# Kernel tuning notes

Measured on AMD Instinct MI355X. Metric: run time of the kernel, lower is better.

## Reference

```python
import jax, jax.numpy as jnp
import numpy as np

# Production-scale dims (see shape_source)
L, H, W = 8, 1536, 1536            # layers, grid height, grid width
C = 12                              # number of inter-layer connections
MAX_DIST, TAU = 5, 2.0              # LocalConnectivity distance kernel
DECAY, THRESH, BETA = 0.9, 0.0, 10.0  # SpikeNode params (decay_rate, spike_threshold, surrogate_beta)

# fixed connection topology (src_layer -> dst_layer), mirrors init connections list
_PAIRS = [(0,1),(1,2),(2,3),(3,4),(4,5),(5,6),(6,7),(0,2),(2,4),(4,6),(7,0),(3,5)]


def _distance_kernel():
    ks = 2 * MAX_DIST + 1
    yy, xx = np.meshgrid(np.arange(ks) - MAX_DIST, np.arange(ks) - MAX_DIST, indexing='ij')
    dist = np.sqrt(yy.astype(np.float64) ** 2 + xx.astype(np.float64) ** 2)
    kern = np.exp(-dist / TAU)
    kern[dist > MAX_DIST] = 0.0
    kern[MAX_DIST, MAX_DIST] = 0.0  # no self-connection
    return jnp.asarray(kern, jnp.float32)


def setup_inputs() -> dict:
    key = jax.random.key(0)
    k1, k2, k3, k4, k5 = jax.random.split(key, 5)
    external = jax.random.normal(k1, (L, H, W), jnp.float32)
    prev_spikes = (jax.random.uniform(k2, (L, H, W)) < 0.1).astype(jnp.float32)
    membrane = jax.random.normal(k3, (L, H, W), jnp.float32) * 0.5
    refractory = jax.random.randint(k4, (L, H, W), 0, 4).astype(jnp.int32)
    inter_weights = jax.random.normal(k5, (C, H, W), jnp.float32) * 0.1
    conn_src = jnp.asarray([p[0] for p in _PAIRS], jnp.int32)
    conn_dst = jnp.asarray([p[1] for p in _PAIRS], jnp.int32)
    return {
        'external': external,
        'prev_spikes': prev_spikes,
        'membrane': membrane,
        'inter_weights': inter_weights,
        'local_kernel': _distance_kernel(),
        'refractory': refractory,
        'conn_src': conn_src,
        'conn_dst': conn_dst,
    }


def reference(external, prev_spikes, membrane, inter_weights, local_kernel,
              refractory, conn_src, conn_dst):
    # --- LocalConnectivity: distance-decay lateral conv on previous spikes ---
    # treat L as batch, single channel; SAME padding keeps [L,H,W]
    internal = jax.lax.conv_general_dilated(
        prev_spikes[:, None, :, :], local_kernel[None, None, :, :],
        window_strides=(1, 1), padding='SAME')[:, 0]

    # --- inter-layer axonal input: sum over connections into each dst layer ---
    contrib = prev_spikes[conn_src] * inter_weights          # [C,H,W]
    axonal = jax.ops.segment_sum(contrib, conn_dst, num_segments=L)  # [L,H,W]

    # --- SpikeNode single CLK step (LIF + refractory + surrogate spike) ---
    total = external + internal + axonal
    active = (refractory == 0).astype(total.dtype)           # not in refractory period
    v_new = DECAY * membrane + active * total
    surr = jax.nn.sigmoid(BETA * (v_new - THRESH))           # surrogate (for grads)
    hard = (v_new > THRESH).astype(total.dtype)              # hard Heaviside forward
    spikes = (hard + surr - jax.lax.stop_gradient(surr)) * active  # straight-through
    return spikes
```

## Files before the change

kernel.cpp:

```cpp
#include <hip/hip_runtime.h>
#include <cmath>

namespace {

constexpr int L = 8, H = 1536, W = 1536, HW = H * W, C = 12;
constexpr int TWB = 128, TH = 16;
constexpr int LH = TH + 10;
constexpr int LPAD = 8;
constexpr int LCOLS = 148;

__device__ __host__ constexpr int XLO[11]  = {5, 2, 1, 1, 1, 0, 1, 1, 1, 2, 5};
__device__ __host__ constexpr int XHI[11]  = {5, 8, 9, 9, 9,10, 9, 9, 9, 8, 5};
__device__ __host__ constexpr int WOFF[11] = {0, 1, 8,17,26,35,46,55,64,73,80};

__device__ constexpr int CSRC[C] = {0,1,2,3,4,5,6,0,2,4,7,3};
__device__ constexpr int CDST[C] = {1,2,3,4,5,6,7,2,4,6,0,5};

struct Weights { float w[81]; };

__global__ __launch_bounds__(256)
void snn_fast(const float* __restrict__ ext,
              const float* __restrict__ spk,
              const float* __restrict__ mem,
              const float* __restrict__ iw,
              const int*   __restrict__ refr,
              float* __restrict__ out,
              unsigned*    wslist,
              unsigned     cap,
              const Weights wt)
{
    __shared__ float tile[LH][LCOLS];

    const int tx = threadIdx.x;
    const int ty = threadIdx.y;
    const int tid = ty * 32 + tx;
    const int bx = blockIdx.x, by = blockIdx.y, l = blockIdx.z;

    const int gx0 = bx * TWB - LPAD;
    const int gy0 = by * TH - 5;
    const float* sp_l = spk + l * HW;
    for (int idx = tid; idx < LH * 36; idx += 256) {
        const int r    = idx / 36;
        const int slot = idx - r * 36;
        const int gy = gy0 + r;
        const int gx = gx0 + 4 * slot;
        float4 v = make_float4(0.f, 0.f, 0.f, 0.f);
        if ((unsigned)gy < (unsigned)H) {
            const float* src = sp_l + gy * W;
            if (gx >= 0 && gx + 3 < W) {
                v = *(const float4*)(src + gx);
            } else {
                float t0 = 0.f, t1 = 0.f, t2 = 0.f, t3 = 0.f;
                if ((unsigned)(gx + 0) < (unsigned)W) t0 = src[gx + 0];
                if ((unsigned)(gx + 1) < (unsigned)W) t1 = src[gx + 1];
                if ((unsigned)(gx + 2) < (unsigned)W) t2 = src[gx + 2];
                if ((unsigned)(gx + 3) < (unsigned)W) t3 = src[gx + 3];
                v = make_float4(t0, t1, t2, t3);
            }
        }
        *(float4*)&tile[r][4 * slot] = v;
    }
    __syncthreads();

    float acc[2][4] = {{0.f,0.f,0.f,0.f},{0.f,0.f,0.f,0.f}};
    #pragma unroll
    for (int j = 0; j < 12; ++j) {
        const float* row = &tile[ty * 2 + j][0];
        alignas(16) float win[20];
        *(float4*)&win[0]  = *(const float4*)&row[4 * tx + 0];
        *(float4*)&win[4]  = *(const float4*)&row[4 * tx + 4];
        *(float4*)&win[8]  = *(const float4*)&row[4 * tx + 8];
        *(float4*)&win[12] = *(const float4*)&row[4 * tx + 12];
        win[16] = row[4 * tx + 16];
        #pragma unroll
        for (int k = 0; k < 2; ++k) {
            const int dy = j - k;
            if (dy < 0 || dy > 10) continue;
            #pragma unroll
            for (int dx = XLO[dy]; dx <= XHI[dy]; ++dx) {
                const float wv = wt.w[WOFF[dy] + dx - XLO[dy]];
                #pragma unroll
                for (int c = 0; c < 4; ++c)
                    acc[k][c] += wv * win[3 + c + dx];
            }
        }
    }

    const int ox = bx * TWB + 4 * tx;
    #pragma unroll
    for (int k = 0; k < 2; ++k) {
        const int oy   = by * TH + ty * 2 + k;
        const int pidx = oy * W + ox;
        const int gidx = l * HW + pidx;

        const int4   rf4 = *(const int4*)  (refr + gidx);
        const float4 e4  = *(const float4*)(ext  + gidx);
        const float4 m4  = *(const float4*)(mem  + gidx);

        float ax0 = 0.f, ax1 = 0.f, ax2 = 0.f, ax3 = 0.f;
        #pragma unroll
        for (int c = 0; c < C; ++c) {
            if (CDST[c] != l) continue;
            const float4 s4 = *(const float4*)(spk + CSRC[c] * HW + pidx);
            const float4 w4 = *(const float4*)(iw  + c       * HW + pidx);
            ax0 += s4.x * w4.x; ax1 += s4.y * w4.y;
            ax2 += s4.z * w4.z; ax3 += s4.w * w4.w;
        }
        const float ee[4] = {e4.x, e4.y, e4.z, e4.w};
        const float mm[4] = {m4.x, m4.y, m4.z, m4.w};
        const int   rr[4] = {rf4.x, rf4.y, rf4.z, rf4.w};
        const float aa[4] = {ax0, ax1, ax2, ax3};
        float res[4];
        #pragma unroll
        for (int c = 0; c < 4; ++c) {
            const float v = 0.9f * mm[c] + (ee[c] + acc[k][c] + aa[c]);
            res[c] = (rr[c] == 0 && v > 0.f) ? 1.f : 0.f;
            if (rr[c] == 0 && __builtin_expect(fabsf(v) < 1e-3f, 0)) {
                const unsigned idx = atomicAdd(wslist, 1u);
                if (idx < cap) wslist[1 + idx] = (unsigned)(gidx + c);
            }
        }
        *(float4*)(out + gidx) = make_float4(res[0], res[1], res[2], res[3]);
    }
}

__global__ __launch_bounds__(256)
void snn_fixup(const float* __restrict__ ext,
               const float* __restrict__ spk,
               const float* __restrict__ mem,
               const float* __restrict__ iw,
               const float* __restrict__ lk,
               float* __restrict__ out,
               const unsigned* __restrict__ wslist,
               unsigned cap)
{
    const unsigned n = min(wslist[0], cap);
    for (unsigned i = blockIdx.x * blockDim.x + threadIdx.x; i < n;
         i += gridDim.x * blockDim.x) {
        const unsigned gidx = wslist[1 + i];
        const int l    = gidx / HW;
        const int pidx = gidx - l * HW;
        const int oy   = pidx / W;
        const int ox   = pidx - oy * W;

        const float* sp = spk + l * HW;
        double conv = 0.0;
        for (int dy = 0; dy < 11; ++dy) {
            const int yy = oy + dy - 5;
            if ((unsigned)yy >= (unsigned)H) continue;
            for (int dx = 0; dx < 11; ++dx) {
                const int xx = ox + dx - 5;
                if ((unsigned)xx >= (unsigned)W) continue;
                conv += (double)lk[dy * 11 + dx] * (double)sp[yy * W + xx];
            }
        }
        double ax = 0.0;
        #pragma unroll
        for (int c = 0; c < C; ++c)
            if (CDST[c] == l)
                ax += (double)spk[CSRC[c] * HW + pidx] * (double)iw[c * HW + pidx];
        const double tot = ((double)ext[gidx] + conv) + ax;
        const double vd  = 0.9 * (double)mem[gidx] + tot;
        out[gidx] = (vd > 0.0) ? 1.f : 0.f;
    }
}

}

extern "C" void kernel_launch(void* const* d_in, const int* in_sizes, int n_in,
                              void* d_out, int out_size, void* d_ws, size_t ws_size,
                              hipStream_t stream) {
    const float* ext  = (const float*)d_in[0];
    const float* spk  = (const float*)d_in[1];
    const float* mem  = (const float*)d_in[2];
    const float* iw   = (const float*)d_in[3];
    const float* lk   = (const float*)d_in[4];
    const int*   refr = (const int*)  d_in[5];
    float* o = (float*)d_out;

    Weights wt;
    for (int dy = 0; dy < 11; ++dy) {
        for (int dx = XLO[dy]; dx <= XHI[dy]; ++dx) {
            const double ddy = dy - 5, ddx = dx - 5;
            const double dist = std::sqrt(ddy * ddy + ddx * ddx);
            double w = std::exp(-dist / 2.0);
            if (dist > 5.0) w = 0.0;
            if (dy == 5 && dx == 5) w = 0.0;
            wt.w[WOFF[dy] + dx - XLO[dy]] = (float)w;
        }
    }

    dim3 grid(W / TWB, H / TH, L);
    dim3 block(32, 8, 1);

    unsigned* wsl = (unsigned*)d_ws;
    size_t cap64 = ws_size / 4 - 1;
    const unsigned cap = (unsigned)(cap64 > 0x7FFFFFFFu ? 0x7FFFFFFFu : cap64);
    hipMemsetAsync(d_ws, 0, 4, stream);
    hipLaunchKernelGGL(snn_fast, grid, block, 0, stream,
                       ext, spk, mem, iw, refr, o, wsl, cap, wt);
    hipLaunchKernelGGL(snn_fixup, dim3(64), dim3(256), 0, stream,
                       ext, spk, mem, iw, lk, o, wsl, cap);
}
```

Measured before the change: 188.8 us.

## Compute lateral convolution with bf16 MFMA using hi/lo split weights

Replaces the scalar FP32 11x11 stencil with matrix-core MFMA instructions. Spike tiles are stored as bf16, which is exact for binary spikes, and the kernel weights are split into bf16 high and low parts to keep near-fp32 accuracy. Each block builds banded Toeplitz B matrices in shared memory from the kernel input, and results pass through LDS for the elementwise epilogue. Tiles shrink to 64x16 with one output float4 per thread, which adds per-block weight-setup cost and more halo overhead.

```diff
diff --git a/kernel.cpp b/kernel.cpp
--- a/kernel.cpp
+++ b/kernel.cpp
@@ -1,127 +1,146 @@
 #include <hip/hip_runtime.h>
+#include <hip/hip_bf16.h>
 #include <cmath>
 
 namespace {
 
 constexpr int L = 8, H = 1536, W = 1536, HW = H * W, C = 12;
-constexpr int TWB = 128, TH = 16;
-constexpr int LH = TH + 10;
-constexpr int LPAD = 8;
-constexpr int LCOLS = 148;
-
-__device__ __host__ constexpr int XLO[11]  = {5, 2, 1, 1, 1, 0, 1, 1, 1, 2, 5};
-__device__ __host__ constexpr int XHI[11]  = {5, 8, 9, 9, 9,10, 9, 9, 9, 8, 5};
-__device__ __host__ constexpr int WOFF[11] = {0, 1, 8,17,26,35,46,55,64,73,80};
+constexpr int BTW = 64, BTH = 16;
+constexpr int TROWS = 26;
+constexpr int TCOLS = 88;
+constexpr int NS4 = 22;
 
 __device__ constexpr int CSRC[C] = {0,1,2,3,4,5,6,0,2,4,7,3};
 __device__ constexpr int CDST[C] = {1,2,3,4,5,6,7,2,4,6,0,5};
 
-struct Weights { float w[81]; };
+typedef __attribute__((ext_vector_type(8))) short bf16x8;
+typedef __attribute__((ext_vector_type(4))) float f32x4;
+
+__device__ __forceinline__ short f2b(float x) {
+    __hip_bfloat16 h = __float2bfloat16(x);
+    return *(short*)&h;
+}
 
 __global__ __launch_bounds__(256)
 void snn_fast(const float* __restrict__ ext,
               const float* __restrict__ spk,
               const float* __restrict__ mem,
               const float* __restrict__ iw,
+              const float* __restrict__ lk,
               const int*   __restrict__ refr,
               float* __restrict__ out,
               unsigned*    wslist,
-              unsigned     cap,
-              const Weights wt)
+              unsigned     cap)
 {
-    __shared__ float tile[LH][LCOLS];
-
-    const int tx = threadIdx.x;
-    const int ty = threadIdx.y;
-    const int tid = ty * 32 + tx;
+    __shared__ short Bhi[11 * 512];
+    __shared__ short Blo[11 * 512];
+    __shared__ short tile[TROWS * TCOLS];
+    __shared__ float accb[4 * 256];
+
+    const int tid = threadIdx.x;
+    const int wv  = tid >> 6;
+    const int ln  = tid & 63;
     const int bx = blockIdx.x, by = blockIdx.y, l = blockIdx.z;
 
-    const int gx0 = bx * TWB - LPAD;
-    const int gy0 = by * TH - 5;
+    for (int i = tid; i < 11 * 512; i += 256) {
+        const int dy   = i >> 9;
+        const int r    = i & 511;
+        const int lane = r >> 3, e = r & 7;
+        const int n = lane & 15;
+        const int k = ((lane >> 4) << 3) + e;
+        const int dx = k - n - 3;
+        float w = 0.f;
+        if (dx >= 0 && dx <= 10) w = lk[dy * 11 + dx];
+        const __hip_bfloat16 hb = __float2bfloat16(w);
+        const float rest = w - __bfloat162float(hb);
+        Bhi[i] = *(const short*)&hb;
+        Blo[i] = f2b(rest);
+    }
+
+    const int gx0 = bx * BTW - 8;
+    const int gy0 = by * BTH - 5;
     const float* sp_l = spk + l * HW;
-    for (int idx = tid; idx < LH * 36; idx += 256) {
-        const int r    = idx / 36;
-        const int slot = idx - r * 36;
-        const int gy = gy0 + r;
-        const int gx = gx0 + 4 * slot;
+    for (int i = tid; i < TROWS * NS4; i += 256) {
+        const int r = i / NS4, s = i - r * NS4;
+        const int gy = gy0 + r, gx = gx0 + 4 * s;
         float4 v = make_float4(0.f, 0.f, 0.f, 0.f);
         if ((unsigned)gy < (unsigned)H) {
             const float* src = sp_l + gy * W;
             if (gx >= 0 && gx + 3 < W) {
                 v = *(const float4*)(src + gx);
             } else {
-                float t0 = 0.f, t1 = 0.f, t2 = 0.f, t3 = 0.f;
-                if ((unsigned)(gx + 0) < (unsigned)W) t0 = src[gx + 0];
-                if ((unsigned)(gx + 1) < (unsigned)W) t1 = src[gx + 1];
-                if ((unsigned)(gx + 2) < (unsigned)W) t2 = src[gx + 2];
-                if ((unsigned)(gx + 3) < (unsigned)W) t3 = src[gx + 3];
-                v = make_float4(t0, t1, t2, t3);
+                if ((unsigned)(gx + 0) < (unsigned)W) v.x = src[gx + 0];
+                if ((unsigned)(gx + 1) < (unsigned)W) v.y = src[gx + 1];
+                if ((unsigned)(gx + 2) < (unsigned)W) v.z = src[gx + 2];
+                if ((unsigned)(gx + 3) < (unsigned)W) v.w = src[gx + 3];
             }
         }
-        *(float4*)&tile[r][4 * slot] = v;
+        short4 b4;
+        b4.x = f2b(v.x); b4.y = f2b(v.y); b4.z = f2b(v.z); b4.w = f2b(v.w);
+        *(short4*)&tile[r * TCOLS + 4 * s] = b4;
     }
     __syncthreads();
 
-    float acc[2][4] = {{0.f,0.f,0.f,0.f},{0.f,0.f,0.f,0.f}};
+    const int m = ln & 15, g = ln >> 4;
+    const short* aptr = tile + m * TCOLS + wv * 16 + g * 8;
+    const short* bhp  = Bhi + ln * 8;
+    const short* blp  = Blo + ln * 8;
+    f32x4 acc = {0.f, 0.f, 0.f, 0.f};
+    #pragma unroll 1
+    for (int dy = 0; dy < 11; ++dy) {
+        const bf16x8 a  = *(const bf16x8*)(aptr + dy * TCOLS);
+        const bf16x8 bh = *(const bf16x8*)(bhp + dy * 512);
+        const bf16x8 bl = *(const bf16x8*)(blp + dy * 512);
+        acc = __builtin_amdgcn_mfma_f32_16x16x32_bf16(a, bh, acc, 0, 0, 0);
+        acc = __builtin_amdgcn_mfma_f32_16x16x32_bf16(a, bl, acc, 0, 0, 0);
+    }
+
+    {
+        float* aw = accb + wv * 256;
+        #pragma unroll
+        for (int r = 0; r < 4; ++r)
+            aw[(g * 4 + r) * 16 + m] = acc[r];
+    }
+    __syncthreads();
+
+    const int trow = ln >> 2;
+    const int tc4  = (ln & 3) * 4;
+    const int oy   = by * BTH + trow;
+    const int ox   = bx * BTW + wv * 16 + tc4;
+    const int pidx = oy * W + ox;
+    const int gidx = l * HW + pidx;
+
+    const f32x4 cv = *(const f32x4*)(accb + wv * 256 + trow * 16 + tc4);
+
+    const int4   rf4 = *(const int4*)  (refr + gidx);
+    const float4 e4  = *(const float4*)(ext  + gidx);
+    const float4 m4  = *(const float4*)(mem  + gidx);
+
+    float ax0 = 0.f, ax1 = 0.f, ax2 = 0.f, ax3 = 0.f;
     #pragma unroll
-    for (int j = 0; j < 12; ++j) {
-        const float* row = &tile[ty * 2 + j][0];
-        alignas(16) float win[20];
-        *(float4*)&win[0]  = *(const float4*)&row[4 * tx + 0];
-        *(float4*)&win[4]  = *(const float4*)&row[4 * tx + 4];
-        *(float4*)&win[8]  = *(const float4*)&row[4 * tx + 8];
-        *(float4*)&win[12] = *(const float4*)&row[4 * tx + 12];
-        win[16] = row[4 * tx + 16];
-        #pragma unroll
-        for (int k = 0; k < 2; ++k) {
-            const int dy = j - k;
-            if (dy < 0 || dy > 10) continue;
-            #pragma unroll
-            for (int dx = XLO[dy]; dx <= XHI[dy]; ++dx) {
-                const float wv = wt.w[WOFF[dy] + dx - XLO[dy]];
-                #pragma unroll
-                for (int c = 0; c < 4; ++c)
-                    acc[k][c] += wv * win[3 + c + dx];
-            }
+    for (int c = 0; c < C; ++c) {
+        if (CDST[c] != l) continue;
+        const float4 s4 = *(const float4*)(spk + CSRC[c] * HW + pidx);
+        const float4 w4 = *(const float4*)(iw  + c       * HW + pidx);
+        ax0 += s4.x * w4.x; ax1 += s4.y * w4.y;
+        ax2 += s4.z * w4.z; ax3 += s4.w * w4.w;
+    }
+    const float ee[4] = {e4.x, e4.y, e4.z, e4.w};
+    const float mm[4] = {m4.x, m4.y, m4.z, m4.w};
+    const int   rr[4] = {rf4.x, rf4.y, rf4.z, rf4.w};
+    const float aa[4] = {ax0, ax1, ax2, ax3};
+    float res[4];
+    #pragma unroll
+    for (int c = 0; c < 4; ++c) {
+        const float v = fmaf(0.9f, mm[c], ee[c] + cv[c] + aa[c]);
+        const bool act = (rr[c] == 0);
+        res[c] = (act && v > 0.f) ? 1.f : 0.f;
+        if (act && __builtin_expect(fabsf(v) < 1e-3f, 0)) {
+            const unsigned idx = atomicAdd(wslist, 1u);
+            if (idx < cap) wslist[1 + idx] = (unsigned)(gidx + c);
         }
     }
-
-    const int ox = bx * TWB + 4 * tx;
-    #pragma unroll
-    for (int k = 0; k < 2; ++k) {
-        const int oy   = by * TH + ty * 2 + k;
-        const int pidx = oy * W + ox;
-        const int gidx = l * HW + pidx;
-
-        const int4   rf4 = *(const int4*)  (refr + gidx);
-        const float4 e4  = *(const float4*)(ext  + gidx);
-        const float4 m4  = *(const float4*)(mem  + gidx);
-
-        float ax0 = 0.f, ax1 = 0.f, ax2 = 0.f, ax3 = 0.f;
-        #pragma unroll
-        for (int c = 0; c < C; ++c) {
-            if (CDST[c] != l) continue;
-            const float4 s4 = *(const float4*)(spk + CSRC[c] * HW + pidx);
-            const float4 w4 = *(const float4*)(iw  + c       * HW + pidx);
-            ax0 += s4.x * w4.x; ax1 += s4.y * w4.y;
-            ax2 += s4.z * w4.z; ax3 += s4.w * w4.w;
-        }
-        const float ee[4] = {e4.x, e4.y, e4.z, e4.w};
-        const float mm[4] = {m4.x, m4.y, m4.z, m4.w};
-        const int   rr[4] = {rf4.x, rf4.y, rf4.z, rf4.w};
-        const float aa[4] = {ax0, ax1, ax2, ax3};
-        float res[4];
-        #pragma unroll
-        for (int c = 0; c < 4; ++c) {
-            const float v = 0.9f * mm[c] + (ee[c] + acc[k][c] + aa[c]);
-            res[c] = (rr[c] == 0 && v > 0.f) ? 1.f : 0.f;
-            if (rr[c] == 0 && __builtin_expect(fabsf(v) < 1e-3f, 0)) {
-                const unsigned idx = atomicAdd(wslist, 1u);
-                if (idx < cap) wslist[1 + idx] = (unsigned)(gidx + c);
-            }
-        }
-        *(float4*)(out + gidx) = make_float4(res[0], res[1], res[2], res[3]);
-    }
+    *(float4*)(out + gidx) = make_float4(res[0], res[1], res[2], res[3]);
 }
 
 __global__ __launch_bounds__(256)
@@ -178,27 +197,15 @@
     const int*   refr = (const int*)  d_in[5];
     float* o = (float*)d_out;
 
-    Weights wt;
-    for (int dy = 0; dy < 11; ++dy) {
-        for (int dx = XLO[dy]; dx <= XHI[dy]; ++dx) {
-            const double ddy = dy - 5, ddx = dx - 5;
-            const double dist = std::sqrt(ddy * ddy + ddx * ddx);
-            double w = std::exp(-dist / 2.0);
-            if (dist > 5.0) w = 0.0;
-            if (dy == 5 && dx == 5) w = 0.0;
-            wt.w[WOFF[dy] + dx - XLO[dy]] = (float)w;
-        }
-    }
-
-    dim3 grid(W / TWB, H / TH, L);
-    dim3 block(32, 8, 1);
+    dim3 grid(W / BTW, H / BTH, L);
+    dim3 block(256, 1, 1);
 
     unsigned* wsl = (unsigned*)d_ws;
     size_t cap64 = ws_size / 4 - 1;
     const unsigned cap = (unsigned)(cap64 > 0x7FFFFFFFu ? 0x7FFFFFFFu : cap64);
     hipMemsetAsync(d_ws, 0, 4, stream);
     hipLaunchKernelGGL(snn_fast, grid, block, 0, stream,
-                       ext, spk, mem, iw, refr, o, wsl, cap, wt);
+                       ext, spk, mem, iw, lk, refr, o, wsl, cap);
     hipLaunchKernelGGL(snn_fixup, dim3(64), dim3(256), 0, stream,
                        ext, spk, mem, iw, lk, o, wsl, cap);
 }
```

Result: slower. 243.1 us (+28.7%).
